# Kernel tuning notes

Hardware: AMD Instinct MI355X
Metric: run time of the kernel (lower is better)

The kernel has to match this reference:

```python
import jax, jax.numpy as jnp
import numpy as np

N = 20000      # nodes
E = 320000     # edges (avg degree 16)
NODE_DIM = 64
EDGE_DIM = 32
HID = 128
HEADS = 4
NEG_SLOPE = 0.2


def _gatv2(x, src, dst, edge_attr, Wl, bl, Wr, br, We, att, bias, heads, out_ch):
    """PyG GATv2Conv (concat=True). x:[N,F], src/dst:[E], edge_attr:[E,edge_dim]."""
    n = x.shape[0]
    xl = (x @ Wl + bl).reshape(n, heads, out_ch)          # source transform
    xr = (x @ Wr + br).reshape(n, heads, out_ch)          # target transform
    ee = (edge_attr @ We).reshape(-1, heads, out_ch)      # edge embedding (no bias in PyG)
    m = jax.nn.leaky_relu(xl[src] + xr[dst] + ee, NEG_SLOPE)  # [E,H,C]
    logits = jnp.einsum('ehc,hc->eh', m, att)             # [E,H]
    # segment softmax over incoming edges of each destination node
    lmax = jax.ops.segment_max(logits, dst, num_segments=n)
    ex = jnp.exp(logits - lmax[dst])
    denom = jax.ops.segment_sum(ex, dst, num_segments=n)
    alpha = ex / denom[dst]                               # [E,H]
    out = jax.ops.segment_sum(alpha[..., None] * xl[src], dst, num_segments=n)
    return out.reshape(n, heads * out_ch) + bias


def setup_inputs() -> dict:
    key = jax.random.key(0)
    ks = jax.random.split(key, 24)
    d = {}
    d['x'] = jax.random.normal(ks[0], (N, NODE_DIM), jnp.float32)
    d['edge_index'] = jax.random.randint(ks[1], (2, E), 0, N, jnp.int64)
    d['edge_attr'] = jax.random.normal(ks[2], (E, EDGE_DIM), jnp.float32)
    HC1 = HEADS * HID
    def lin(k, fi, fo):
        return jax.random.normal(k, (fi, fo), jnp.float32) / np.sqrt(fi).astype(np.float32)
    # conv1: node_dim -> hid, heads=4
    d['Wl1'] = lin(ks[3], NODE_DIM, HC1); d['bl1'] = jnp.zeros((HC1,), jnp.float32)
    d['Wr1'] = lin(ks[4], NODE_DIM, HC1); d['br1'] = jnp.zeros((HC1,), jnp.float32)
    d['We1'] = lin(ks[5], EDGE_DIM, HC1)
    d['att1'] = jax.random.normal(ks[6], (HEADS, HID), jnp.float32) / np.sqrt(HID).astype(np.float32)
    d['bias1'] = jnp.zeros((HC1,), jnp.float32)
    # conv2: hid*heads -> hid, heads=1
    d['Wl2'] = lin(ks[7], HC1, HID); d['bl2'] = jnp.zeros((HID,), jnp.float32)
    d['Wr2'] = lin(ks[8], HC1, HID); d['br2'] = jnp.zeros((HID,), jnp.float32)
    d['We2'] = lin(ks[9], EDGE_DIM, HID)
    d['att2'] = jax.random.normal(ks[10], (1, HID), jnp.float32) / np.sqrt(HID).astype(np.float32)
    d['bias2'] = jnp.zeros((HID,), jnp.float32)
    # stereo head
    d['Wh1'] = lin(ks[11], HID, 64); d['bh1'] = jnp.zeros((64,), jnp.float32)
    d['Wh2'] = lin(ks[12], 64, 2);   d['bh2'] = jnp.zeros((2,), jnp.float32)
    return d


def reference(x, edge_index, edge_attr, Wl1, bl1, Wr1, br1, We1, att1, bias1,
              Wl2, bl2, Wr2, br2, We2, att2, bias2, Wh1, bh1, Wh2, bh2):
    src, dst = edge_index[0], edge_index[1]
    h = _gatv2(x, src, dst, edge_attr, Wl1, bl1, Wr1, br1, We1, att1, bias1, HEADS, HID)
    h = jax.nn.relu(h)
    h = _gatv2(h, src, dst, edge_attr, Wl2, bl2, Wr2, br2, We2, att2, bias2, 1, HID)
    h = jax.nn.relu(h @ Wh1 + bh1)
    return h @ Wh2 + bh2  # [N, 2]
```

## Files before the change

kernel.cpp:

```cpp
#include <hip/hip_runtime.h>
#include <hip/hip_bf16.h>
#include <math.h>

#define N_NODES 20000
#define N_EDGES 320000
#define NODE_DIM 64
#define EDGE_DIM 32
#define HID 128
#define HEADS 4
#define HC1 512
#define NEG_SLOPE 0.2f

typedef __attribute__((ext_vector_type(8))) short bf16x8;
typedef __attribute__((ext_vector_type(4))) float f32x4;

__device__ __forceinline__ unsigned short f2b(float f) {
  __hip_bfloat16 h = __float2bfloat16(f);
  unsigned short s;
  __builtin_memcpy(&s, &h, 2);
  return s;
}
__device__ __forceinline__ float b2f(unsigned short b) {
  return __uint_as_float(((unsigned)b) << 16);
}

__global__ void deg_count_kernel(const int* __restrict__ dsts, int* __restrict__ deg) {
  int e = blockIdx.x * blockDim.x + threadIdx.x;
  if (e < N_EDGES) atomicAdd(&deg[dsts[e]], 1);
}

__global__ __launch_bounds__(1024) void scan_kernel(
    const int* __restrict__ deg, int* __restrict__ offs, int* __restrict__ cursor)
{
  __shared__ int part[1024];
  int t = threadIdx.x;
  const int C = 20;
  int base = t * C;
  int loc[C]; int s = 0;
  #pragma unroll
  for (int i = 0; i < C; i++) { loc[i] = s; int idx = base + i; s += (idx < N_NODES) ? deg[idx] : 0; }
  part[t] = s;
  __syncthreads();
  for (int off = 1; off < 1024; off <<= 1) {
    int v = (t >= off) ? part[t - off] : 0;
    __syncthreads();
    part[t] += v;
    __syncthreads();
  }
  int pbase = (t > 0) ? part[t - 1] : 0;
  #pragma unroll
  for (int i = 0; i < C; i++) {
    int idx = base + i;
    if (idx < N_NODES) { int o = pbase + loc[i]; offs[idx] = o; cursor[idx] = o; }
  }
  if (t == 1023) offs[N_NODES] = part[1023];
}

__global__ void scatter_kernel(const int* __restrict__ dsts, int* __restrict__ cursor,
                               int* __restrict__ csr) {
  int e = blockIdx.x * blockDim.x + threadIdx.x;
  if (e >= N_EDGES) return;
  int pos = atomicAdd(&cursor[dsts[e]], 1);
  csr[pos] = e;
}

__global__ void wconv_kernel(const float* __restrict__ Wl1, const float* __restrict__ Wr1,
                             const float* __restrict__ Wl2, const float* __restrict__ Wr2,
                             unsigned short* __restrict__ WT1, unsigned short* __restrict__ WT2)
{
  int i = blockIdx.x * blockDim.x + threadIdx.x;
  if (i < 1024 * 64) {
    int col = i >> 6, k = i & 63;
    float v = (col < 512) ? Wl1[(size_t)k * HC1 + col] : Wr1[(size_t)k * HC1 + col - 512];
    WT1[i] = f2b(v);
  }
  if (i < 256 * 512) {
    int col = i >> 9, k = i & 511;
    float v = (col < 128) ? Wl2[(size_t)k * HID + col] : Wr2[(size_t)k * HID + col - 128];
    WT2[i] = f2b(v);
  }
}

__global__ __launch_bounds__(256, 4) void linear1_kernel(
    const float* __restrict__ x, const unsigned short* __restrict__ WT1,
    const float* __restrict__ bl, const float* __restrict__ br,
    unsigned short* __restrict__ xlb, float* __restrict__ xr)
{
  __shared__ short xs[16 * 72];
  int t = threadIdx.x;
  int n0 = blockIdx.x * 16;
  {
    int i = t * 4;
    int node = i >> 6, k = i & 63;
    float4 v = *(const float4*)&x[(size_t)(n0 + node) * NODE_DIM + k];
    short* d = &xs[node * 72 + k];
    d[0] = (short)f2b(v.x); d[1] = (short)f2b(v.y);
    d[2] = (short)f2b(v.z); d[3] = (short)f2b(v.w);
  }
  __syncthreads();
  int wave = t >> 6, lane = t & 63;
  int l15 = lane & 15, l16 = lane >> 4;
  bf16x8 a0 = *(bf16x8*)&xs[l15 * 72 + 0  + l16 * 8];
  bf16x8 a1 = *(bf16x8*)&xs[l15 * 72 + 32 + l16 * 8];
  #pragma unroll 4
  for (int tt = 0; tt < 16; tt++) {
    int col = wave * 256 + tt * 16 + l15;
    const unsigned short* wp = &WT1[(size_t)col * 64 + l16 * 8];
    bf16x8 b0 = *(bf16x8*)&wp[0];
    bf16x8 b1 = *(bf16x8*)&wp[32];
    f32x4 acc = {0.f, 0.f, 0.f, 0.f};
    acc = __builtin_amdgcn_mfma_f32_16x16x32_bf16(a0, b0, acc, 0, 0, 0);
    acc = __builtin_amdgcn_mfma_f32_16x16x32_bf16(a1, b1, acc, 0, 0, 0);
    if (col < 512) {
      float bv = bl[col];
      #pragma unroll
      for (int r = 0; r < 4; r++)
        xlb[(size_t)(n0 + l16 * 4 + r) * HC1 + col] = f2b(acc[r] + bv);
    } else {
      float bv = br[col - 512];
      #pragma unroll
      for (int r = 0; r < 4; r++)
        xr[(size_t)(n0 + l16 * 4 + r) * HC1 + col - 512] = acc[r] + bv;
    }
  }
}

__global__ __launch_bounds__(512, 2) void fused1_kernel(
    const float* __restrict__ ea, const int* __restrict__ srcs,
    const float* __restrict__ We, const float* __restrict__ att,
    const unsigned short* __restrict__ xlb, const float* __restrict__ xr,
    const float* __restrict__ bias, const int* __restrict__ offs,
    const int* __restrict__ csr, unsigned short* __restrict__ h1b)
{
  __shared__ short WtT[256 * 40];
  __shared__ short easb[8][16 * 40];
  __shared__ short ee_b[8][8][264];
  int t = threadIdx.x;
  int half = blockIdx.x & 1;
  for (int i = t; i < EDGE_DIM * 256; i += 512) {
    int k = i >> 8, c = i & 255;
    WtT[c * 40 + k] = (short)f2b(We[(size_t)k * HC1 + half * 256 + c]);
  }
  __syncthreads();
  int wave = t >> 6, lane = t & 63;
  int l15 = lane & 15, l16 = lane >> 4;
  int n = (blockIdx.x >> 1) * 8 + wave;
  int Cl = lane * 4;
  int C = half * 256 + Cl;
  float at4[4], xr4[4];
  *(float4*)at4 = *(const float4*)&att[C];
  *(float4*)xr4 = *(const float4*)&xr[(size_t)n * HC1 + C];
  float o4[4] = {0.f,0.f,0.f,0.f};
  float mx = 8.0f, dn = 0.f;
  int beg = offs[n], end = offs[n + 1];
  int ev = 0, sv = 0;
  if (lane < 8 && beg + lane < end) { ev = csr[beg + lane]; sv = srcs[ev]; }
  for (int i0 = beg; i0 < end; i0 += 8) {
    int nv = end - i0; if (nv > 8) nv = 8;
    int sarr[8];
    #pragma unroll
    for (int j = 0; j < 8; j++) sarr[j] = __shfl(sv, j);
    float xv[8][4];
    #pragma unroll
    for (int j = 0; j < 8; j++) {
      if (j < nv) {
        ushort4 u = *(const ushort4*)&xlb[(size_t)sarr[j] * HC1 + C];
        xv[j][0] = b2f(u.x); xv[j][1] = b2f(u.y);
        xv[j][2] = b2f(u.z); xv[j][3] = b2f(u.w);
      } else { xv[j][0] = 0.f; xv[j][1] = 0.f; xv[j][2] = 0.f; xv[j][3] = 0.f; }
    }
    {
      int me = __shfl(ev, lane >> 2);
      if (lane < 32) {
        int q = lane & 3;
        float4 u0 = *(const float4*)&ea[(size_t)me * EDGE_DIM + q * 8];
        float4 u1 = *(const float4*)&ea[(size_t)me * EDGE_DIM + q * 8 + 4];
        short* dst = &easb[wave][(lane >> 2) * 40 + q * 8];
        dst[0] = (short)f2b(u0.x); dst[1] = (short)f2b(u0.y);
        dst[2] = (short)f2b(u0.z); dst[3] = (short)f2b(u0.w);
        dst[4] = (short)f2b(u1.x); dst[5] = (short)f2b(u1.y);
        dst[6] = (short)f2b(u1.z); dst[7] = (short)f2b(u1.w);
      }
    }
    if (lane < 8 && i0 + 8 + lane < end) { ev = csr[i0 + 8 + lane]; sv = srcs[ev]; }
    bf16x8 bfrag = *(bf16x8*)&easb[wave][l15 * 40 + l16 * 8];
    #pragma unroll 4
    for (int tt = 0; tt < 16; tt++) {
      bf16x8 afrag = *(bf16x8*)&WtT[(tt * 16 + l15) * 40 + l16 * 8];
      f32x4 cz = {0.f, 0.f, 0.f, 0.f};
      f32x4 cv = __builtin_amdgcn_mfma_f32_16x16x32_bf16(afrag, bfrag, cz, 0, 0, 0);
      if (l15 < 8) {
        ushort4 u;
        u.x = f2b(cv[0]); u.y = f2b(cv[1]); u.z = f2b(cv[2]); u.w = f2b(cv[3]);
        *(ushort4*)&ee_b[wave][l15][tt * 16 + l16 * 4] = u;
      }
    }
    float pl[8];
    #pragma unroll
    for (int j = 0; j < 8; j++) {
      ushort4 ub = *(const ushort4*)&ee_b[wave][j][Cl];
      float z0 = b2f(ub.x) + xv[j][0] + xr4[0];
      float z1 = b2f(ub.y) + xv[j][1] + xr4[1];
      float z2 = b2f(ub.z) + xv[j][2] + xr4[2];
      float z3 = b2f(ub.w) + xv[j][3] + xr4[3];
      z0 = z0 > 0.f ? z0 : NEG_SLOPE * z0;
      z1 = z1 > 0.f ? z1 : NEG_SLOPE * z1;
      z2 = z2 > 0.f ? z2 : NEG_SLOPE * z2;
      z3 = z3 > 0.f ? z3 : NEG_SLOPE * z3;
      float s = ((z0 * at4[0] + z1 * at4[1]) + (z2 * at4[2] + z3 * at4[3]));
      #pragma unroll
      for (int o = 1; o <= 16; o <<= 1) s += __shfl_xor(s, o);
      pl[j] = (j < nv) ? s : -3.0e38f;
    }
    float cm = fmaxf(fmaxf(fmaxf(pl[0], pl[1]), fmaxf(pl[2], pl[3])),
                     fmaxf(fmaxf(pl[4], pl[5]), fmaxf(pl[6], pl[7])));
    float mn = fmaxf(mx, cm);
    if (__any(mn > mx + 8.f)) {
      float fs = __expf(mx - mn);
      dn *= fs;
      #pragma unroll
      for (int c = 0; c < 4; c++) o4[c] *= fs;
      mx = mn;
    }
    float p[8];
    #pragma unroll
    for (int j = 0; j < 8; j++) p[j] = __expf(pl[j] - mx);
    dn += ((p[0] + p[1]) + (p[2] + p[3])) + ((p[4] + p[5]) + (p[6] + p[7]));
    #pragma unroll
    for (int c = 0; c < 4; c++) {
      float acc = 0.f;
      #pragma unroll
      for (int j = 0; j < 8; j++) acc = fmaf(p[j], xv[j][c], acc);
      o4[c] += acc;
    }
  }
  float iv = dn > 0.f ? 1.f / dn : 0.f;
  ushort4 u;
  float v0 = o4[0] * iv + bias[C + 0]; v0 = v0 > 0.f ? v0 : 0.f;
  float v1 = o4[1] * iv + bias[C + 1]; v1 = v1 > 0.f ? v1 : 0.f;
  float v2 = o4[2] * iv + bias[C + 2]; v2 = v2 > 0.f ? v2 : 0.f;
  float v3 = o4[3] * iv + bias[C + 3]; v3 = v3 > 0.f ? v3 : 0.f;
  u.x = f2b(v0); u.y = f2b(v1); u.z = f2b(v2); u.w = f2b(v3);
  *(ushort4*)&h1b[(size_t)n * HC1 + C] = u;
}

__global__ __launch_bounds__(256, 4) void linear2_kernel(
    const unsigned short* __restrict__ hin, const unsigned short* __restrict__ WT2,
    const float* __restrict__ bl, const float* __restrict__ br,
    unsigned short* __restrict__ xlb2, float* __restrict__ xr2)
{
  __shared__ short hs[16 * 520];
  int t = threadIdx.x;
  int n0 = blockIdx.x * 16;
  for (int rr = 0; rr < 8; rr++) {
    int i = (t + rr * 256) * 4;
    int node = i >> 9, k = i & 511;
    short* d = &hs[node * 520 + k];
    ushort4 u = *(const ushort4*)&hin[(size_t)(n0 + node) * HC1 + k];
    d[0] = (short)u.x; d[1] = (short)u.y; d[2] = (short)u.z; d[3] = (short)u.w;
  }
  __syncthreads();
  int wave = t >> 6, lane = t & 63;
  int l15 = lane & 15, l16 = lane >> 4;
  f32x4 acc0 = {0.f,0.f,0.f,0.f}, acc1 = {0.f,0.f,0.f,0.f};
  f32x4 acc2 = {0.f,0.f,0.f,0.f}, acc3 = {0.f,0.f,0.f,0.f};
  int colb = wave * 64 + l15;
  #pragma unroll 2
  for (int ks = 0; ks < 16; ks++) {
    bf16x8 a = *(bf16x8*)&hs[l15 * 520 + ks * 32 + l16 * 8];
    bf16x8 b0 = *(bf16x8*)&WT2[(size_t)(colb +  0) * 512 + ks * 32 + l16 * 8];
    bf16x8 b1 = *(bf16x8*)&WT2[(size_t)(colb + 16) * 512 + ks * 32 + l16 * 8];
    bf16x8 b2 = *(bf16x8*)&WT2[(size_t)(colb + 32) * 512 + ks * 32 + l16 * 8];
    bf16x8 b3 = *(bf16x8*)&WT2[(size_t)(colb + 48) * 512 + ks * 32 + l16 * 8];
    acc0 = __builtin_amdgcn_mfma_f32_16x16x32_bf16(a, b0, acc0, 0, 0, 0);
    acc1 = __builtin_amdgcn_mfma_f32_16x16x32_bf16(a, b1, acc1, 0, 0, 0);
    acc2 = __builtin_amdgcn_mfma_f32_16x16x32_bf16(a, b2, acc2, 0, 0, 0);
    acc3 = __builtin_amdgcn_mfma_f32_16x16x32_bf16(a, b3, acc3, 0, 0, 0);
  }
  #pragma unroll
  for (int tt = 0; tt < 4; tt++) {
    const f32x4* ap = (tt == 0) ? &acc0 : (tt == 1) ? &acc1 : (tt == 2) ? &acc2 : &acc3;
    int col = wave * 64 + tt * 16 + l15;
    if (col < 128) {
      float bv = bl[col];
      #pragma unroll
      for (int r = 0; r < 4; r++)
        xlb2[(size_t)(n0 + l16 * 4 + r) * HID + col] = f2b((*ap)[r] + bv);
    } else {
      float bv = br[col - 128];
      #pragma unroll
      for (int r = 0; r < 4; r++)
        xr2[(size_t)(n0 + l16 * 4 + r) * HID + col - 128] = (*ap)[r] + bv;
    }
  }
}

__global__ __launch_bounds__(512, 2) void fused2_kernel(
    const float* __restrict__ ea, const int* __restrict__ srcs,
    const float* __restrict__ We, const float* __restrict__ att,
    const unsigned short* __restrict__ xlb2, const float* __restrict__ xr,
    const float* __restrict__ bias, const int* __restrict__ offs,
    const int* __restrict__ csr, float* __restrict__ h2out)
{
  __shared__ short W2tT[HID * 40];
  __shared__ short easb2[8][16 * 40];
  __shared__ short ee2b[8][16][136];
  int t = threadIdx.x;
  for (int i = t; i < EDGE_DIM * HID; i += 512) {
    int k = i >> 7, c = i & 127;
    W2tT[c * 40 + k] = (short)f2b(We[(size_t)k * HID + c]);
  }
  __syncthreads();
  int wave = t >> 6, lane = t & 63;
  int l15 = lane & 15, l16 = lane >> 4;
  int n = blockIdx.x * 8 + wave;
  int c = lane * 2;
  float2 atv = *(const float2*)&att[c];
  float2 xrv = *(const float2*)&xr[(size_t)n * HID + c];
  float oa = 0.f, ob = 0.f;
  float m = 8.0f, d = 0.f;
  int beg = offs[n], end = offs[n + 1];
  int ev = 0, sv = 0;
  if (lane < 16 && beg + lane < end) { ev = csr[beg + lane]; sv = srcs[ev]; }
  for (int i0 = beg; i0 < end; i0 += 16) {
    int nv = end - i0; if (nv > 16) nv = 16;
    int sarr[16];
    #pragma unroll
    for (int j = 0; j < 16; j++) sarr[j] = __shfl(sv, j);
    float2 xv[16];
    #pragma unroll
    for (int j = 0; j < 16; j++) {
      if (j < nv) {
        ushort2 u = *(const ushort2*)&xlb2[(size_t)sarr[j] * HID + c];
        xv[j].x = b2f(u.x); xv[j].y = b2f(u.y);
      } else { xv[j].x = 0.f; xv[j].y = 0.f; }
    }
    {
      int me = __shfl(ev, lane >> 2);
      int q = lane & 3;
      float4 u0 = *(const float4*)&ea[(size_t)me * EDGE_DIM + q * 8];
      float4 u1 = *(const float4*)&ea[(size_t)me * EDGE_DIM + q * 8 + 4];
      short* dst = &easb2[wave][(lane >> 2) * 40 + q * 8];
      dst[0] = (short)f2b(u0.x); dst[1] = (short)f2b(u0.y);
      dst[2] = (short)f2b(u0.z); dst[3] = (short)f2b(u0.w);
      dst[4] = (short)f2b(u1.x); dst[5] = (short)f2b(u1.y);
      dst[6] = (short)f2b(u1.z); dst[7] = (short)f2b(u1.w);
    }
    if (lane < 16 && i0 + 16 + lane < end) { ev = csr[i0 + 16 + lane]; sv = srcs[ev]; }
    bf16x8 bfrag = *(bf16x8*)&easb2[wave][l15 * 40 + l16 * 8];
    #pragma unroll 4
    for (int tt = 0; tt < 8; tt++) {
      bf16x8 afrag = *(bf16x8*)&W2tT[(tt * 16 + l15) * 40 + l16 * 8];
      f32x4 cz = {0.f, 0.f, 0.f, 0.f};
      f32x4 cv = __builtin_amdgcn_mfma_f32_16x16x32_bf16(afrag, bfrag, cz, 0, 0, 0);
      ushort4 u;
      u.x = f2b(cv[0]); u.y = f2b(cv[1]); u.z = f2b(cv[2]); u.w = f2b(cv[3]);
      *(ushort4*)&ee2b[wave][l15][tt * 16 + l16 * 4] = u;
    }
    float pl[16];
    #pragma unroll
    for (int j = 0; j < 16; j++) {
      ushort2 uv = *(const ushort2*)&ee2b[wave][j][c];
      float za = b2f(uv.x) + xv[j].x + xrv.x;
      float zb = b2f(uv.y) + xv[j].y + xrv.y;
      za = za > 0.f ? za : NEG_SLOPE * za;
      zb = zb > 0.f ? zb : NEG_SLOPE * zb;
      float s = za * atv.x + zb * atv.y;
      #pragma unroll
      for (int o = 1; o < 64; o <<= 1) s += __shfl_xor(s, o);
      pl[j] = (j < nv) ? s : -3.0e38f;
    }
    float cm = pl[0];
    #pragma unroll
    for (int j = 1; j < 16; j++) cm = fmaxf(cm, pl[j]);
    float mn = fmaxf(m, cm);
    if (__any(mn > m + 8.f)) {
      float fs = __expf(m - mn);
      d *= fs; oa *= fs; ob *= fs;
      m = mn;
    }
    #pragma unroll
    for (int j = 0; j < 16; j++) {
      float p = __expf(pl[j] - m);
      d += p;
      oa = fmaf(p, xv[j].x, oa);
      ob = fmaf(p, xv[j].y, ob);
    }
  }
  float invd = d > 0.f ? 1.f / d : 0.f;
  float2 o2 = make_float2(oa * invd + bias[c], ob * invd + bias[c + 1]);
  *(float2*)&h2out[(size_t)n * HID + c] = o2;
}

__global__ __launch_bounds__(256) void head_kernel(
    const float* __restrict__ h2, const float* __restrict__ Wh1,
    const float* __restrict__ bh1, const float* __restrict__ Wh2,
    const float* __restrict__ bh2, float* __restrict__ out)
{
  __shared__ float hs[16][HID];
  __shared__ float ts[16][64];
  int n0 = blockIdx.x * 16;
  int t = threadIdx.x;
  for (int r = 0; r < 2; r++) {
    int flat = (t + r * 256) * 4;
    int i = flat >> 7, k = flat & 127;
    *(float4*)&hs[i][k] = *(const float4*)&h2[(size_t)(n0 + i) * HID + k];
  }
  __syncthreads();
  int j = t & 63, g = t >> 6;
  float acc[4];
  #pragma unroll
  for (int q = 0; q < 4; q++) acc[q] = 0.f;
  for (int k = 0; k < HID; k++) {
    float w = Wh1[k * 64 + j];
    #pragma unroll
    for (int q = 0; q < 4; q++) acc[q] = fmaf(hs[g + 4 * q][k], w, acc[q]);
  }
  float bj = bh1[j];
  #pragma unroll
  for (int q = 0; q < 4; q++) {
    float v = acc[q] + bj;
    ts[g + 4 * q][j] = v > 0.f ? v : 0.f;
  }
  __syncthreads();
  if (t < 32) {
    int nl = t >> 1, k = t & 1;
    float acc2 = bh2[k];
    for (int jj = 0; jj < 64; jj++) acc2 = fmaf(ts[nl][jj], Wh2[jj * 2 + k], acc2);
    out[(size_t)(n0 + nl) * 2 + k] = acc2;
  }
}

extern "C" void kernel_launch(void* const* d_in, const int* in_sizes, int n_in,
                              void* d_out, int out_size, void* d_ws, size_t ws_size,
                              hipStream_t stream)
{
  (void)in_sizes; (void)n_in; (void)out_size; (void)ws_size;
  const float* x    = (const float*)d_in[0];
  const int* eidx   = (const int*)d_in[1];
  const float* ea   = (const float*)d_in[2];
  const float* Wl1  = (const float*)d_in[3];
  const float* bl1  = (const float*)d_in[4];
  const float* Wr1  = (const float*)d_in[5];
  const float* br1  = (const float*)d_in[6];
  const float* We1  = (const float*)d_in[7];
  const float* att1 = (const float*)d_in[8];
  const float* bias1= (const float*)d_in[9];
  const float* Wl2  = (const float*)d_in[10];
  const float* bl2  = (const float*)d_in[11];
  const float* Wr2  = (const float*)d_in[12];
  const float* br2  = (const float*)d_in[13];
  const float* We2  = (const float*)d_in[14];
  const float* att2 = (const float*)d_in[15];
  const float* bias2= (const float*)d_in[16];
  const float* Wh1  = (const float*)d_in[17];
  const float* bh1  = (const float*)d_in[18];
  const float* Wh2  = (const float*)d_in[19];
  const float* bh2  = (const float*)d_in[20];
  const int* srcs = eidx;
  const int* dsts = eidx + N_EDGES;
  float* out = (float*)d_out;

  char* p = (char*)d_ws;
  auto alloc = [&](size_t bytes) { char* q = p; p += (bytes + 511) & ~(size_t)511; return q; };
  unsigned short* xlb1 = (unsigned short*)alloc((size_t)N_NODES * HC1 * 2);
  float*          xr1  = (float*)alloc((size_t)N_NODES * HC1 * 4);
  unsigned short* h1b  = (unsigned short*)alloc((size_t)N_NODES * HC1 * 2);
  unsigned short* xlb2 = (unsigned short*)alloc((size_t)N_NODES * HID * 2);
  float*          xr2  = (float*)alloc((size_t)N_NODES * HID * 4);
  float*          h2   = (float*)alloc((size_t)N_NODES * HID * 4);
  int* deg    = (int*)alloc((size_t)N_NODES * 4);
  int* offs   = (int*)alloc((size_t)(N_NODES + 1) * 4);
  int* cursor = (int*)alloc((size_t)N_NODES * 4);
  int* csr    = (int*)alloc((size_t)N_EDGES * 4);
  unsigned short* WT1 = (unsigned short*)alloc(1024 * 64 * 2);
  unsigned short* WT2 = (unsigned short*)alloc(256 * 512 * 2);

  hipMemsetAsync(deg, 0, (size_t)N_NODES * 4, stream);
  hipLaunchKernelGGL(deg_count_kernel, dim3((N_EDGES + 255) / 256), dim3(256), 0, stream, dsts, deg);
  hipLaunchKernelGGL(wconv_kernel, dim3(512), dim3(256), 0, stream, Wl1, Wr1, Wl2, Wr2, WT1, WT2);
  hipLaunchKernelGGL(scan_kernel, dim3(1), dim3(1024), 0, stream, deg, offs, cursor);
  hipLaunchKernelGGL(scatter_kernel, dim3((N_EDGES + 255) / 256), dim3(256), 0, stream, dsts, cursor, csr);
  hipLaunchKernelGGL(linear1_kernel, dim3(N_NODES / 16), dim3(256), 0, stream,
                     x, WT1, bl1, br1, xlb1, xr1);
  hipLaunchKernelGGL(fused1_kernel, dim3((N_NODES / 8) * 2), dim3(512), 0, stream,
                     ea, srcs, We1, att1, xlb1, xr1, bias1, offs, csr, h1b);
  hipLaunchKernelGGL(linear2_kernel, dim3(N_NODES / 16), dim3(256), 0, stream,
                     h1b, WT2, bl2, br2, xlb2, xr2);
  hipLaunchKernelGGL(fused2_kernel, dim3(N_NODES / 8), dim3(512), 0, stream,
                     ea, srcs, We2, att2, xlb2, xr2, bias2, offs, csr, h2);
  hipLaunchKernelGGL(head_kernel, dim3(N_NODES / 16), dim3(256), 0, stream,
                     h2, Wh1, bh1, Wh2, bh2, out);
}
```

Measured before the change: 458.7 us.

## Store xl in fp32, widen fused1 to 16 waves, split edge-embedding staging

Both linear kernels now write the source transform xl in fp32 rather than bf16, and the fused kernels gather fp32 rows directly. This removes the conversion step and gains precision, but doubles the bytes moved in the gather. fused1 now runs 1024 threads covering 16 nodes per block. The per-wave edge-embedding buffer is halved by computing it in two 128-column phases, with lanes split between the phases. Layer-2 buffers are aliased into the xl1 allocation to shrink the workspace.

```diff
diff --git a/kernel.cpp b/kernel.cpp
--- a/kernel.cpp
+++ b/kernel.cpp
@@ -84,7 +84,7 @@
 __global__ __launch_bounds__(256, 4) void linear1_kernel(
     const float* __restrict__ x, const unsigned short* __restrict__ WT1,
     const float* __restrict__ bl, const float* __restrict__ br,
-    unsigned short* __restrict__ xlb, float* __restrict__ xr)
+    float* __restrict__ xl, float* __restrict__ xr)
 {
   __shared__ short xs[16 * 72];
   int t = threadIdx.x;
@@ -111,42 +111,39 @@
     f32x4 acc = {0.f, 0.f, 0.f, 0.f};
     acc = __builtin_amdgcn_mfma_f32_16x16x32_bf16(a0, b0, acc, 0, 0, 0);
     acc = __builtin_amdgcn_mfma_f32_16x16x32_bf16(a1, b1, acc, 0, 0, 0);
-    if (col < 512) {
-      float bv = bl[col];
-      #pragma unroll
-      for (int r = 0; r < 4; r++)
-        xlb[(size_t)(n0 + l16 * 4 + r) * HC1 + col] = f2b(acc[r] + bv);
-    } else {
-      float bv = br[col - 512];
-      #pragma unroll
-      for (int r = 0; r < 4; r++)
-        xr[(size_t)(n0 + l16 * 4 + r) * HC1 + col - 512] = acc[r] + bv;
-    }
-  }
-}
-
-__global__ __launch_bounds__(512, 2) void fused1_kernel(
+    float bv = (col < 512) ? bl[col] : br[col - 512];
+    float* outp = (col < 512) ? xl : xr;
+    int cc = (col < 512) ? col : col - 512;
+    #pragma unroll
+    for (int r = 0; r < 4; r++)
+      outp[(size_t)(n0 + l16 * 4 + r) * HC1 + cc] = acc[r] + bv;
+  }
+}
+
+__global__ __launch_bounds__(1024, 2) void fused1_kernel(
     const float* __restrict__ ea, const int* __restrict__ srcs,
     const float* __restrict__ We, const float* __restrict__ att,
-    const unsigned short* __restrict__ xlb, const float* __restrict__ xr,
+    const float* __restrict__ xl, const float* __restrict__ xr,
     const float* __restrict__ bias, const int* __restrict__ offs,
     const int* __restrict__ csr, unsigned short* __restrict__ h1b)
 {
   __shared__ short WtT[256 * 40];
-  __shared__ short easb[8][16 * 40];
-  __shared__ short ee_b[8][8][264];
+  __shared__ short easb[16][16 * 40];
+  __shared__ short ee_b[16][8][136];
   int t = threadIdx.x;
   int half = blockIdx.x & 1;
-  for (int i = t; i < EDGE_DIM * 256; i += 512) {
+  for (int i = t; i < EDGE_DIM * 256; i += 1024) {
     int k = i >> 8, c = i & 255;
     WtT[c * 40 + k] = (short)f2b(We[(size_t)k * HC1 + half * 256 + c]);
   }
   __syncthreads();
   int wave = t >> 6, lane = t & 63;
   int l15 = lane & 15, l16 = lane >> 4;
-  int n = (blockIdx.x >> 1) * 8 + wave;
+  int n = (blockIdx.x >> 1) * 16 + wave;
   int Cl = lane * 4;
   int C = half * 256 + Cl;
+  bool phA = (Cl < 128);
+  int Cm = Cl & 127;
   float at4[4], xr4[4];
   *(float4*)at4 = *(const float4*)&att[C];
   *(float4*)xr4 = *(const float4*)&xr[(size_t)n * HC1 + C];
@@ -163,11 +160,8 @@
     float xv[8][4];
     #pragma unroll
     for (int j = 0; j < 8; j++) {
-      if (j < nv) {
-        ushort4 u = *(const ushort4*)&xlb[(size_t)sarr[j] * HC1 + C];
-        xv[j][0] = b2f(u.x); xv[j][1] = b2f(u.y);
-        xv[j][2] = b2f(u.z); xv[j][3] = b2f(u.w);
-      } else { xv[j][0] = 0.f; xv[j][1] = 0.f; xv[j][2] = 0.f; xv[j][3] = 0.f; }
+      if (j < nv) *(float4*)&xv[j][0] = *(const float4*)&xl[(size_t)sarr[j] * HC1 + C];
+      else { xv[j][0] = 0.f; xv[j][1] = 0.f; xv[j][2] = 0.f; xv[j][3] = 0.f; }
     }
     {
       int me = __shfl(ev, lane >> 2);
@@ -184,8 +178,9 @@
     }
     if (lane < 8 && i0 + 8 + lane < end) { ev = csr[i0 + 8 + lane]; sv = srcs[ev]; }
     bf16x8 bfrag = *(bf16x8*)&easb[wave][l15 * 40 + l16 * 8];
+    float pl[8];
     #pragma unroll 4
-    for (int tt = 0; tt < 16; tt++) {
+    for (int tt = 0; tt < 8; tt++) {
       bf16x8 afrag = *(bf16x8*)&WtT[(tt * 16 + l15) * 40 + l16 * 8];
       f32x4 cz = {0.f, 0.f, 0.f, 0.f};
       f32x4 cv = __builtin_amdgcn_mfma_f32_16x16x32_bf16(afrag, bfrag, cz, 0, 0, 0);
@@ -195,19 +190,52 @@
         *(ushort4*)&ee_b[wave][l15][tt * 16 + l16 * 4] = u;
       }
     }
-    float pl[8];
     #pragma unroll
     for (int j = 0; j < 8; j++) {
-      ushort4 ub = *(const ushort4*)&ee_b[wave][j][Cl];
-      float z0 = b2f(ub.x) + xv[j][0] + xr4[0];
-      float z1 = b2f(ub.y) + xv[j][1] + xr4[1];
-      float z2 = b2f(ub.z) + xv[j][2] + xr4[2];
-      float z3 = b2f(ub.w) + xv[j][3] + xr4[3];
-      z0 = z0 > 0.f ? z0 : NEG_SLOPE * z0;
-      z1 = z1 > 0.f ? z1 : NEG_SLOPE * z1;
-      z2 = z2 > 0.f ? z2 : NEG_SLOPE * z2;
-      z3 = z3 > 0.f ? z3 : NEG_SLOPE * z3;
-      float s = ((z0 * at4[0] + z1 * at4[1]) + (z2 * at4[2] + z3 * at4[3]));
+      float s = 0.f;
+      if (phA) {
+        ushort4 ub = *(const ushort4*)&ee_b[wave][j][Cm];
+        float z0 = b2f(ub.x) + xv[j][0] + xr4[0];
+        float z1 = b2f(ub.y) + xv[j][1] + xr4[1];
+        float z2 = b2f(ub.z) + xv[j][2] + xr4[2];
+        float z3 = b2f(ub.w) + xv[j][3] + xr4[3];
+        z0 = z0 > 0.f ? z0 : NEG_SLOPE * z0;
+        z1 = z1 > 0.f ? z1 : NEG_SLOPE * z1;
+        z2 = z2 > 0.f ? z2 : NEG_SLOPE * z2;
+        z3 = z3 > 0.f ? z3 : NEG_SLOPE * z3;
+        s = ((z0 * at4[0] + z1 * at4[1]) + (z2 * at4[2] + z3 * at4[3]));
+      }
+      pl[j] = s;
+    }
+    #pragma unroll 4
+    for (int tt = 8; tt < 16; tt++) {
+      bf16x8 afrag = *(bf16x8*)&WtT[(tt * 16 + l15) * 40 + l16 * 8];
+      f32x4 cz = {0.f, 0.f, 0.f, 0.f};
+      f32x4 cv = __builtin_amdgcn_mfma_f32_16x16x32_bf16(afrag, bfrag, cz, 0, 0, 0);
+      if (l15 < 8) {
+        ushort4 u;
+        u.x = f2b(cv[0]); u.y = f2b(cv[1]); u.z = f2b(cv[2]); u.w = f2b(cv[3]);
+        *(ushort4*)&ee_b[wave][l15][(tt - 8) * 16 + l16 * 4] = u;
+      }
+    }
+    #pragma unroll
+    for (int j = 0; j < 8; j++) {
+      if (!phA) {
+        ushort4 ub = *(const ushort4*)&ee_b[wave][j][Cm];
+        float z0 = b2f(ub.x) + xv[j][0] + xr4[0];
+        float z1 = b2f(ub.y) + xv[j][1] + xr4[1];
+        float z2 = b2f(ub.z) + xv[j][2] + xr4[2];
+        float z3 = b2f(ub.w) + xv[j][3] + xr4[3];
+        z0 = z0 > 0.f ? z0 : NEG_SLOPE * z0;
+        z1 = z1 > 0.f ? z1 : NEG_SLOPE * z1;
+        z2 = z2 > 0.f ? z2 : NEG_SLOPE * z2;
+        z3 = z3 > 0.f ? z3 : NEG_SLOPE * z3;
+        pl[j] = ((z0 * at4[0] + z1 * at4[1]) + (z2 * at4[2] + z3 * at4[3]));
+      }
+    }
+    #pragma unroll
+    for (int j = 0; j < 8; j++) {
+      float s = pl[j];
       #pragma unroll
       for (int o = 1; o <= 16; o <<= 1) s += __shfl_xor(s, o);
       pl[j] = (j < nv) ? s : -3.0e38f;
@@ -247,7 +275,7 @@
 __global__ __launch_bounds__(256, 4) void linear2_kernel(
     const unsigned short* __restrict__ hin, const unsigned short* __restrict__ WT2,
     const float* __restrict__ bl, const float* __restrict__ br,
-    unsigned short* __restrict__ xlb2, float* __restrict__ xr2)
+    float* __restrict__ xl2, float* __restrict__ xr2)
 {
   __shared__ short hs[16 * 520];
   int t = threadIdx.x;
@@ -281,24 +309,19 @@
   for (int tt = 0; tt < 4; tt++) {
     const f32x4* ap = (tt == 0) ? &acc0 : (tt == 1) ? &acc1 : (tt == 2) ? &acc2 : &acc3;
     int col = wave * 64 + tt * 16 + l15;
-    if (col < 128) {
-      float bv = bl[col];
-      #pragma unroll
-      for (int r = 0; r < 4; r++)
-        xlb2[(size_t)(n0 + l16 * 4 + r) * HID + col] = f2b((*ap)[r] + bv);
-    } else {
-      float bv = br[col - 128];
-      #pragma unroll
-      for (int r = 0; r < 4; r++)
-        xr2[(size_t)(n0 + l16 * 4 + r) * HID + col - 128] = (*ap)[r] + bv;
-    }
+    float bv = (col < 128) ? bl[col] : br[col - 128];
+    float* outp = (col < 128) ? xl2 : xr2;
+    int cc = (col < 128) ? col : col - 128;
+    #pragma unroll
+    for (int r = 0; r < 4; r++)
+      outp[(size_t)(n0 + l16 * 4 + r) * HID + cc] = (*ap)[r] + bv;
   }
 }
 
 __global__ __launch_bounds__(512, 2) void fused2_kernel(
     const float* __restrict__ ea, const int* __restrict__ srcs,
     const float* __restrict__ We, const float* __restrict__ att,
-    const unsigned short* __restrict__ xlb2, const float* __restrict__ xr,
+    const float* __restrict__ xl, const float* __restrict__ xr,
     const float* __restrict__ bias, const int* __restrict__ offs,
     const int* __restrict__ csr, float* __restrict__ h2out)
 {
@@ -330,10 +353,8 @@
     float2 xv[16];
     #pragma unroll
     for (int j = 0; j < 16; j++) {
-      if (j < nv) {
-        ushort2 u = *(const ushort2*)&xlb2[(size_t)sarr[j] * HID + c];
-        xv[j].x = b2f(u.x); xv[j].y = b2f(u.y);
-      } else { xv[j].x = 0.f; xv[j].y = 0.f; }
+      if (j < nv) xv[j] = *(const float2*)&xl[(size_t)sarr[j] * HID + c];
+      else { xv[j].x = 0.f; xv[j].y = 0.f; }
     }
     {
       int me = __shfl(ev, lane >> 2);
@@ -463,18 +484,18 @@
 
   char* p = (char*)d_ws;
   auto alloc = [&](size_t bytes) { char* q = p; p += (bytes + 511) & ~(size_t)511; return q; };
-  unsigned short* xlb1 = (unsigned short*)alloc((size_t)N_NODES * HC1 * 2);
+  float*          xl1  = (float*)alloc((size_t)N_NODES * HC1 * 4);
   float*          xr1  = (float*)alloc((size_t)N_NODES * HC1 * 4);
   unsigned short* h1b  = (unsigned short*)alloc((size_t)N_NODES * HC1 * 2);
-  unsigned short* xlb2 = (unsigned short*)alloc((size_t)N_NODES * HID * 2);
-  float*          xr2  = (float*)alloc((size_t)N_NODES * HID * 4);
-  float*          h2   = (float*)alloc((size_t)N_NODES * HID * 4);
   int* deg    = (int*)alloc((size_t)N_NODES * 4);
   int* offs   = (int*)alloc((size_t)(N_NODES + 1) * 4);
   int* cursor = (int*)alloc((size_t)N_NODES * 4);
   int* csr    = (int*)alloc((size_t)N_EDGES * 4);
   unsigned short* WT1 = (unsigned short*)alloc(1024 * 64 * 2);
   unsigned short* WT2 = (unsigned short*)alloc(256 * 512 * 2);
+  float* xl2 = xl1;
+  float* xr2 = xl1 + (size_t)N_NODES * HID;
+  float* h2  = xl1 + (size_t)2 * N_NODES * HID;
 
   hipMemsetAsync(deg, 0, (size_t)N_NODES * 4, stream);
   hipLaunchKernelGGL(deg_count_kernel, dim3((N_EDGES + 255) / 256), dim3(256), 0, stream, dsts, deg);
@@ -482,13 +503,13 @@
   hipLaunchKernelGGL(scan_kernel, dim3(1), dim3(1024), 0, stream, deg, offs, cursor);
   hipLaunchKernelGGL(scatter_kernel, dim3((N_EDGES + 255) / 256), dim3(256), 0, stream, dsts, cursor, csr);
   hipLaunchKernelGGL(linear1_kernel, dim3(N_NODES / 16), dim3(256), 0, stream,
-                     x, WT1, bl1, br1, xlb1, xr1);
-  hipLaunchKernelGGL(fused1_kernel, dim3((N_NODES / 8) * 2), dim3(512), 0, stream,
-                     ea, srcs, We1, att1, xlb1, xr1, bias1, offs, csr, h1b);
+                     x, WT1, bl1, br1, xl1, xr1);
+  hipLaunchKernelGGL(fused1_kernel, dim3((N_NODES / 16) * 2), dim3(1024), 0, stream,
+                     ea, srcs, We1, att1, xl1, xr1, bias1, offs, csr, h1b);
   hipLaunchKernelGGL(linear2_kernel, dim3(N_NODES / 16), dim3(256), 0, stream,
-                     h1b, WT2, bl2, br2, xlb2, xr2);
+                     h1b, WT2, bl2, br2, xl2, xr2);
   hipLaunchKernelGGL(fused2_kernel, dim3(N_NODES / 8), dim3(512), 0, stream,
-                     ea, srcs, We2, att2, xlb2, xr2, bias2, offs, csr, h2);
+                     ea, srcs, We2, att2, xl2, xr2, bias2, offs, csr, h2);
   hipLaunchKernelGGL(head_kernel, dim3(N_NODES / 16), dim3(256), 0, stream,
                      h2, Wh1, bh1, Wh2, bh2, out);
 }
```

Result: faster. 411.1 us (-10.4%).
